# Optimization experiments

Measured on AMD Instinct MI355X. Metric: run time of the kernel, lower is better.

Reference implementation:

```python
import jax, jax.numpy as jnp
import numpy as np

EPS = 1e-12

def l2_normalize(x, axis=-1):
    return x * jax.lax.rsqrt(jnp.sum(x * x, axis=axis, keepdims=True) + EPS)

def setup_inputs() -> dict:
    key = jax.random.key(0)
    k1, k2 = jax.random.split(key)
    hidden_states = jax.random.normal(k1, (32, 1024, 32), dtype=jnp.float32)
    embedding = jax.random.normal(k2, (8192, 32), dtype=jnp.float32)
    return {"hidden_states": hidden_states, "embedding": embedding}

def reference(hidden_states, embedding):
    B, N, D = hidden_states.shape
    # flatten to tokens and L2-normalize both sides
    z_flat = l2_normalize(hidden_states.reshape(-1, D), axis=1)      # [B*N, D]
    emb_n = l2_normalize(embedding, axis=1)                          # [K, D]
    # pairwise squared L2 distance (on normalized vectors)
    distance = (jnp.sum(z_flat ** 2, axis=1, keepdims=True)
                + jnp.sum(emb_n ** 2, axis=1)
                - 2.0 * jnp.dot(z_flat, emb_n.T))                    # [B*N, K]
    min_encoding_indices = jnp.argmin(distance, axis=1).reshape(B, N)
    # codebook lookup on the RAW embedding, then normalize (get_codebook_entry)
    z_q = l2_normalize(jnp.take(embedding, min_encoding_indices, axis=0), axis=-1)  # [B, N, D]
    hidden_normed = l2_normalize(hidden_states, axis=-1)
    e_latent_loss = jnp.mean(jnp.square(jax.lax.stop_gradient(z_q) - hidden_normed))
    q_latent_loss = jnp.mean(jnp.square(z_q - jax.lax.stop_gradient(hidden_normed)))
    # straight-through estimator
    z_q = hidden_states + jax.lax.stop_gradient(z_q - hidden_states)
    return (z_q, min_encoding_indices, q_latent_loss, e_latent_loss)
```

## Files before the change

kernel.cpp:

```cpp
#include <hip/hip_runtime.h>
#include <math.h>

#define TOKENS 32768
#define KCODES 8192
#define DIM 32
#define CHUNKS 8
#define CPC (KCODES / CHUNKS)
#define ZQ_ELEMS (TOKENS * DIM)

typedef __attribute__((ext_vector_type(8))) short short8v;
typedef __attribute__((ext_vector_type(4))) float f32x4;

__device__ inline unsigned rne16(unsigned u) {
  return (u + 0x7FFFu + ((u >> 16) & 1u)) >> 16;
}

__global__ __launch_bounds__(256) void prep_codes(
    const float* __restrict__ emb, short* __restrict__ cA,
    short* __restrict__ cB, short* __restrict__ cC, float* __restrict__ nsq) {
  int gid = blockIdx.x * 256 + threadIdx.x;
  int code = gid >> 5;
  int k = gid & 31;
  float v = emb[gid];
  float s = v * v;
#pragma unroll
  for (int off = 16; off > 0; off >>= 1) s += __shfl_xor(s, off, 32);
  float r = 1.0f / sqrtf(s + 1e-12f);
  float en = v * r;
  float s2 = en * en;
#pragma unroll
  for (int off = 16; off > 0; off >>= 1) s2 += __shfl_xor(s2, off, 32);
  if (k == 0) nsq[code] = s2;

  float w = -2.0f * en;
  unsigned ua = rne16(__float_as_uint(w));
  float fa = __uint_as_float(ua << 16);
  float r1 = w - fa;
  unsigned ub = rne16(__float_as_uint(r1));
  float fb = __uint_as_float(ub << 16);
  float r2 = r1 - fb;
  unsigned uc = rne16(__float_as_uint(r2));

  int tile = code >> 4;
  int lane = (code & 15) | ((k >> 3) << 4);
  int off = tile * 512 + lane * 8 + (k & 7);
  cA[off] = (short)ua;
  cB[off] = (short)ub;
  cC[off] = (short)uc;
}

__global__ __launch_bounds__(256) void argmin_mfma(
    const float* __restrict__ hs, const short* __restrict__ cA,
    const short* __restrict__ cB, const short* __restrict__ cC,
    const float* __restrict__ nsqG, float* __restrict__ pdist,
    int* __restrict__ pidx) {
  __shared__ short lA[4096];
  __shared__ short lB[4096];
  __shared__ short lC[4096];
  __shared__ float lN[128];

  int tid = threadIdx.x;
  int l = tid & 63;
  int w = tid >> 6;
  int g = l >> 4;
  int c16 = l & 15;

  int gt0 = blockIdx.x * 16 + w * 4;

  short8v bA[4], bB[4], bC[4];
#pragma unroll
  for (int tt = 0; tt < 4; tt++) {
    int tok = (gt0 + tt) * 16 + c16;
    const float4* hp4 = (const float4*)(hs + (size_t)tok * DIM + g * 8);
    float4 q0 = hp4[0];
    float4 q1 = hp4[1];
    float x[8] = {q0.x, q0.y, q0.z, q0.w, q1.x, q1.y, q1.z, q1.w};
    float ss = 0.f;
#pragma unroll
    for (int j = 0; j < 8; j++) ss += x[j] * x[j];
    ss += __shfl_xor(ss, 16);
    ss += __shfl_xor(ss, 32);
    float rz = 1.0f / sqrtf(ss + 1e-12f);
#pragma unroll
    for (int j = 0; j < 8; j++) {
      float zn = x[j] * rz;
      unsigned ua = rne16(__float_as_uint(zn));
      float fa = __uint_as_float(ua << 16);
      float r1 = zn - fa;
      unsigned ub = rne16(__float_as_uint(r1));
      float fb = __uint_as_float(ub << 16);
      float r2 = r1 - fb;
      unsigned uc = rne16(__float_as_uint(r2));
      bA[tt][j] = (short)ua;
      bB[tt][j] = (short)ub;
      bC[tt][j] = (short)uc;
    }
  }

  float best[4] = {3.4e38f, 3.4e38f, 3.4e38f, 3.4e38f};
  int bidx[4] = {0, 0, 0, 0};
  int cbase = blockIdx.y * CPC;

  for (int s = 0; s < 8; s++) {
    __syncthreads();
    size_t eb = ((size_t)(cbase >> 4) + s * 8) * 512;
    const float4* sA = (const float4*)(cA + eb);
    const float4* sB = (const float4*)(cB + eb);
    const float4* sC = (const float4*)(cC + eb);
    ((float4*)lA)[tid] = sA[tid];
    ((float4*)lA)[tid + 256] = sA[tid + 256];
    ((float4*)lB)[tid] = sB[tid];
    ((float4*)lB)[tid + 256] = sB[tid + 256];
    ((float4*)lC)[tid] = sC[tid];
    ((float4*)lC)[tid + 256] = sC[tid + 256];
    if (tid < 128) lN[tid] = nsqG[cbase + s * 128 + tid];
    __syncthreads();

#pragma unroll
    for (int ct = 0; ct < 8; ct++) {
      f32x4 nv = *(const f32x4*)&lN[ct * 16 + g * 4];
      short8v aA = *(const short8v*)&lA[ct * 512 + l * 8];
      short8v aB = *(const short8v*)&lB[ct * 512 + l * 8];
      short8v aC = *(const short8v*)&lC[ct * 512 + l * 8];
      f32x4 acc[4];
#pragma unroll
      for (int tt = 0; tt < 4; tt++)
        acc[tt] = __builtin_amdgcn_mfma_f32_16x16x32_bf16(aA, bA[tt], nv, 0, 0, 0);
#pragma unroll
      for (int tt = 0; tt < 4; tt++)
        acc[tt] = __builtin_amdgcn_mfma_f32_16x16x32_bf16(aA, bB[tt], acc[tt], 0, 0, 0);
#pragma unroll
      for (int tt = 0; tt < 4; tt++)
        acc[tt] = __builtin_amdgcn_mfma_f32_16x16x32_bf16(aB, bA[tt], acc[tt], 0, 0, 0);
#pragma unroll
      for (int tt = 0; tt < 4; tt++)
        acc[tt] = __builtin_amdgcn_mfma_f32_16x16x32_bf16(aA, bC[tt], acc[tt], 0, 0, 0);
#pragma unroll
      for (int tt = 0; tt < 4; tt++)
        acc[tt] = __builtin_amdgcn_mfma_f32_16x16x32_bf16(aC, bA[tt], acc[tt], 0, 0, 0);
#pragma unroll
      for (int tt = 0; tt < 4; tt++)
        acc[tt] = __builtin_amdgcn_mfma_f32_16x16x32_bf16(aB, bB[tt], acc[tt], 0, 0, 0);

      int rb = cbase + s * 128 + ct * 16 + g * 4;
#pragma unroll
      for (int tt = 0; tt < 4; tt++) {
#pragma unroll
        for (int r = 0; r < 4; r++) {
          float d = acc[tt][r];
          if (d < best[tt]) { best[tt] = d; bidx[tt] = rb + r; }
        }
      }
    }
  }

#pragma unroll
  for (int tt = 0; tt < 4; tt++) {
    {
      float od = __shfl_xor(best[tt], 16);
      int oi = __shfl_xor(bidx[tt], 16);
      if (od < best[tt] || (od == best[tt] && oi < bidx[tt])) {
        best[tt] = od; bidx[tt] = oi;
      }
    }
    {
      float od = __shfl_xor(best[tt], 32);
      int oi = __shfl_xor(bidx[tt], 32);
      if (od < best[tt] || (od == best[tt] && oi < bidx[tt])) {
        best[tt] = od; bidx[tt] = oi;
      }
    }
    if (l < 16) {
      int tok = (gt0 + tt) * 16 + c16;
      pdist[(size_t)tok * CHUNKS + blockIdx.y] = best[tt];
      pidx[(size_t)tok * CHUNKS + blockIdx.y] = bidx[tt];
    }
  }
}

__global__ __launch_bounds__(256) void finalize_kernel(
    const float* __restrict__ hs, const float* __restrict__ emb,
    const float* __restrict__ pdist, const int* __restrict__ pidx,
    float* __restrict__ out, float* __restrict__ lossacc) {
  int token = blockIdx.x * 256 + threadIdx.x;

  float best = 3.4e38f;
  int bidx = 0;
#pragma unroll
  for (int c = 0; c < CHUNKS; c++) {
    float d = pdist[(size_t)token * CHUNKS + c];
    int i = pidx[(size_t)token * CHUNKS + c];
    if (d < best || (d == best && i < bidx)) { best = d; bidx = i; }
  }
  out[(size_t)ZQ_ELEMS + token] = (float)bidx;

  const float4* e = (const float4*)(emb + (size_t)bidx * DIM);
  float4 ev[8];
  float s = 0.f;
#pragma unroll
  for (int j = 0; j < 8; j++) {
    ev[j] = e[j];
    s += ev[j].x * ev[j].x + ev[j].y * ev[j].y + ev[j].z * ev[j].z +
         ev[j].w * ev[j].w;
  }
  float r = 1.0f / sqrtf(s + 1e-12f);

  const float4* hp = (const float4*)(hs + (size_t)token * DIM);
  float4 hv[8];
  float ss = 0.f;
#pragma unroll
  for (int j = 0; j < 8; j++) {
    hv[j] = hp[j];
    ss += hv[j].x * hv[j].x + hv[j].y * hv[j].y + hv[j].z * hv[j].z +
          hv[j].w * hv[j].w;
  }
  float rz = 1.0f / sqrtf(ss + 1e-12f);

  float4* op = (float4*)(out + (size_t)token * DIM);
  float acc = 0.f;
#pragma unroll
  for (int j = 0; j < 8; j++) {
    float4 zq;
    zq.x = ev[j].x * r; zq.y = ev[j].y * r;
    zq.z = ev[j].z * r; zq.w = ev[j].w * r;
    op[j] = zq;
    float dx = zq.x - hv[j].x * rz;
    float dy = zq.y - hv[j].y * rz;
    float dz = zq.z - hv[j].z * rz;
    float dw = zq.w - hv[j].w * rz;
    acc += dx * dx + dy * dy + dz * dz + dw * dw;
  }

#pragma unroll
  for (int off = 32; off > 0; off >>= 1) acc += __shfl_xor(acc, off, 64);
  __shared__ float red[4];
  int wid = threadIdx.x >> 6;
  if ((threadIdx.x & 63) == 0) red[wid] = acc;
  __syncthreads();
  if (threadIdx.x == 0) {
    float b = red[0] + red[1] + red[2] + red[3];
    atomicAdd(lossacc, b);
  }
}

__global__ void loss_write_kernel(const float* __restrict__ lossacc,
                                  float* __restrict__ out) {
  float l = lossacc[0] * (1.0f / (float)ZQ_ELEMS);
  out[ZQ_ELEMS + TOKENS] = l;
  out[ZQ_ELEMS + TOKENS + 1] = l;
}

extern "C" void kernel_launch(void* const* d_in, const int* in_sizes, int n_in,
                              void* d_out, int out_size, void* d_ws,
                              size_t ws_size, hipStream_t stream) {
  const float* hs = (const float*)d_in[0];
  const float* emb = (const float*)d_in[1];
  float* out = (float*)d_out;
  char* ws = (char*)d_ws;

  short* cA = (short*)(ws);
  short* cB = (short*)(ws + 524288);
  short* cC = (short*)(ws + 1048576);
  float* nsq = (float*)(ws + 1572864);
  float* pdist = (float*)(ws + 1605632);
  int* pidx = (int*)(ws + 2654208);
  float* lossacc = (float*)(ws + 3702784);

  hipLaunchKernelGGL(prep_codes, dim3((KCODES * DIM) / 256), dim3(256), 0,
                     stream, emb, cA, cB, cC, nsq);
  hipLaunchKernelGGL(argmin_mfma, dim3(TOKENS / 256, CHUNKS), dim3(256), 0,
                     stream, hs, cA, cB, cC, nsq, pdist, pidx);
  hipMemsetAsync(lossacc, 0, 4, stream);
  hipLaunchKernelGGL(finalize_kernel, dim3(TOKENS / 256), dim3(256), 0, stream,
                     hs, emb, pdist, pidx, out, lossacc);
  hipLaunchKernelGGL(loss_write_kernel, dim3(1), dim3(1), 0, stream, lossacc,
                     out);
}
```

Before: 102.1 us.

## Screen codes with low-precision MFMA, then rescore candidate groups in double

Replaces the six-pass bf16x3 exact argmin with a cheaper three-MFMA bf16x2 screening pass that records per-group minimum scores per token. A rescore kernel then recomputes exact double-precision distances only for codebook groups within a margin of the best screened score, and fuses the codebook lookup and loss. The screen skips token normalization because it does not change the argmin, and the loss accumulator is split across many addresses to reduce atomic contention. The risk is that the fixed margin may miss the true minimum, and double-precision rescoring per candidate group can be expensive on the vector units.

```diff
diff --git a/kernel.cpp b/kernel.cpp
--- a/kernel.cpp
+++ b/kernel.cpp
@@ -4,9 +4,12 @@
 #define TOKENS 32768
 #define KCODES 8192
 #define DIM 32
-#define CHUNKS 8
-#define CPC (KCODES / CHUNKS)
+#define NCHUNK 16
+#define CPC 512
+#define GSZ 128
+#define NGROUPS 64
 #define ZQ_ELEMS (TOKENS * DIM)
+#define MARGIN 1e-3f
 
 typedef __attribute__((ext_vector_type(8))) short short8v;
 typedef __attribute__((ext_vector_type(4))) float f32x4;
@@ -17,57 +20,40 @@
 
 __global__ __launch_bounds__(256) void prep_codes(
     const float* __restrict__ emb, short* __restrict__ cA,
-    short* __restrict__ cB, short* __restrict__ cC, float* __restrict__ nsq) {
+    short* __restrict__ cB, double* __restrict__ seArr) {
   int gid = blockIdx.x * 256 + threadIdx.x;
   int code = gid >> 5;
   int k = gid & 31;
   float v = emb[gid];
-  float s = v * v;
-#pragma unroll
-  for (int off = 16; off > 0; off >>= 1) s += __shfl_xor(s, off, 32);
-  float r = 1.0f / sqrtf(s + 1e-12f);
-  float en = v * r;
-  float s2 = en * en;
-#pragma unroll
-  for (int off = 16; off > 0; off >>= 1) s2 += __shfl_xor(s2, off, 32);
-  if (k == 0) nsq[code] = s2;
-
-  float w = -2.0f * en;
+  double dv = (double)v;
+  double ds = dv * dv;
+#pragma unroll
+  for (int off = 16; off > 0; off >>= 1) ds += __shfl_xor(ds, off, 32);
+  if (k == 0) seArr[code] = ds;
+  float r = 1.0f / sqrtf((float)ds + 1e-12f);
+  float w = -v * r;
   unsigned ua = rne16(__float_as_uint(w));
   float fa = __uint_as_float(ua << 16);
-  float r1 = w - fa;
-  unsigned ub = rne16(__float_as_uint(r1));
-  float fb = __uint_as_float(ub << 16);
-  float r2 = r1 - fb;
-  unsigned uc = rne16(__float_as_uint(r2));
-
+  unsigned ub = rne16(__float_as_uint(w - fa));
   int tile = code >> 4;
   int lane = (code & 15) | ((k >> 3) << 4);
   int off = tile * 512 + lane * 8 + (k & 7);
   cA[off] = (short)ua;
   cB[off] = (short)ub;
-  cC[off] = (short)uc;
-}
-
-__global__ __launch_bounds__(256) void argmin_mfma(
+}
+
+__global__ __launch_bounds__(256) void screen_kernel(
     const float* __restrict__ hs, const short* __restrict__ cA,
-    const short* __restrict__ cB, const short* __restrict__ cC,
-    const float* __restrict__ nsqG, float* __restrict__ pdist,
-    int* __restrict__ pidx) {
-  __shared__ short lA[4096];
-  __shared__ short lB[4096];
-  __shared__ short lC[4096];
-  __shared__ float lN[128];
-
+    const short* __restrict__ cB, float* __restrict__ pgmin) {
   int tid = threadIdx.x;
   int l = tid & 63;
   int w = tid >> 6;
   int g = l >> 4;
   int c16 = l & 15;
-
   int gt0 = blockIdx.x * 16 + w * 4;
-
-  short8v bA[4], bB[4], bC[4];
+  int chunk = blockIdx.y;
+
+  short8v zA[4], zB[4];
 #pragma unroll
   for (int tt = 0; tt < 4; tt++) {
     int tok = (gt0 + tt) * 16 + c16;
@@ -75,179 +61,148 @@
     float4 q0 = hp4[0];
     float4 q1 = hp4[1];
     float x[8] = {q0.x, q0.y, q0.z, q0.w, q1.x, q1.y, q1.z, q1.w};
-    float ss = 0.f;
-#pragma unroll
-    for (int j = 0; j < 8; j++) ss += x[j] * x[j];
-    ss += __shfl_xor(ss, 16);
-    ss += __shfl_xor(ss, 32);
-    float rz = 1.0f / sqrtf(ss + 1e-12f);
 #pragma unroll
     for (int j = 0; j < 8; j++) {
-      float zn = x[j] * rz;
-      unsigned ua = rne16(__float_as_uint(zn));
+      unsigned ua = rne16(__float_as_uint(x[j]));
       float fa = __uint_as_float(ua << 16);
-      float r1 = zn - fa;
-      unsigned ub = rne16(__float_as_uint(r1));
-      float fb = __uint_as_float(ub << 16);
-      float r2 = r1 - fb;
-      unsigned uc = rne16(__float_as_uint(r2));
-      bA[tt][j] = (short)ua;
-      bB[tt][j] = (short)ub;
-      bC[tt][j] = (short)uc;
-    }
-  }
-
-  float best[4] = {3.4e38f, 3.4e38f, 3.4e38f, 3.4e38f};
-  int bidx[4] = {0, 0, 0, 0};
-  int cbase = blockIdx.y * CPC;
-
-  for (int s = 0; s < 8; s++) {
-    __syncthreads();
-    size_t eb = ((size_t)(cbase >> 4) + s * 8) * 512;
-    const float4* sA = (const float4*)(cA + eb);
-    const float4* sB = (const float4*)(cB + eb);
-    const float4* sC = (const float4*)(cC + eb);
-    ((float4*)lA)[tid] = sA[tid];
-    ((float4*)lA)[tid + 256] = sA[tid + 256];
-    ((float4*)lB)[tid] = sB[tid];
-    ((float4*)lB)[tid + 256] = sB[tid + 256];
-    ((float4*)lC)[tid] = sC[tid];
-    ((float4*)lC)[tid + 256] = sC[tid + 256];
-    if (tid < 128) lN[tid] = nsqG[cbase + s * 128 + tid];
-    __syncthreads();
-
-#pragma unroll
-    for (int ct = 0; ct < 8; ct++) {
-      f32x4 nv = *(const f32x4*)&lN[ct * 16 + g * 4];
-      short8v aA = *(const short8v*)&lA[ct * 512 + l * 8];
-      short8v aB = *(const short8v*)&lB[ct * 512 + l * 8];
-      short8v aC = *(const short8v*)&lC[ct * 512 + l * 8];
-      f32x4 acc[4];
-#pragma unroll
-      for (int tt = 0; tt < 4; tt++)
-        acc[tt] = __builtin_amdgcn_mfma_f32_16x16x32_bf16(aA, bA[tt], nv, 0, 0, 0);
-#pragma unroll
-      for (int tt = 0; tt < 4; tt++)
-        acc[tt] = __builtin_amdgcn_mfma_f32_16x16x32_bf16(aA, bB[tt], acc[tt], 0, 0, 0);
-#pragma unroll
-      for (int tt = 0; tt < 4; tt++)
-        acc[tt] = __builtin_amdgcn_mfma_f32_16x16x32_bf16(aB, bA[tt], acc[tt], 0, 0, 0);
-#pragma unroll
-      for (int tt = 0; tt < 4; tt++)
-        acc[tt] = __builtin_amdgcn_mfma_f32_16x16x32_bf16(aA, bC[tt], acc[tt], 0, 0, 0);
-#pragma unroll
-      for (int tt = 0; tt < 4; tt++)
-        acc[tt] = __builtin_amdgcn_mfma_f32_16x16x32_bf16(aC, bA[tt], acc[tt], 0, 0, 0);
-#pragma unroll
-      for (int tt = 0; tt < 4; tt++)
-        acc[tt] = __builtin_amdgcn_mfma_f32_16x16x32_bf16(aB, bB[tt], acc[tt], 0, 0, 0);
-
-      int rb = cbase + s * 128 + ct * 16 + g * 4;
+      unsigned ub = rne16(__float_as_uint(x[j] - fa));
+      zA[tt][j] = (short)ua;
+      zB[tt][j] = (short)ub;
+    }
+  }
+
+  int tbase = chunk * (CPC / 16);
+
+  for (int grp = 0; grp < CPC / GSZ; grp++) {
+    float gm[4] = {3.4e38f, 3.4e38f, 3.4e38f, 3.4e38f};
+#pragma unroll
+    for (int ct = 0; ct < GSZ / 16; ct++) {
+      int tile = tbase + grp * (GSZ / 16) + ct;
+      short8v aA = *((const short8v*)(cA + (size_t)tile * 512) + l);
+      short8v aB = *((const short8v*)(cB + (size_t)tile * 512) + l);
 #pragma unroll
       for (int tt = 0; tt < 4; tt++) {
-#pragma unroll
-        for (int r = 0; r < 4; r++) {
-          float d = acc[tt][r];
-          if (d < best[tt]) { best[tt] = d; bidx[tt] = rb + r; }
-        }
-      }
-    }
-  }
-
-#pragma unroll
-  for (int tt = 0; tt < 4; tt++) {
-    {
-      float od = __shfl_xor(best[tt], 16);
-      int oi = __shfl_xor(bidx[tt], 16);
-      if (od < best[tt] || (od == best[tt] && oi < bidx[tt])) {
-        best[tt] = od; bidx[tt] = oi;
-      }
-    }
-    {
-      float od = __shfl_xor(best[tt], 32);
-      int oi = __shfl_xor(bidx[tt], 32);
-      if (od < best[tt] || (od == best[tt] && oi < bidx[tt])) {
-        best[tt] = od; bidx[tt] = oi;
-      }
-    }
-    if (l < 16) {
-      int tok = (gt0 + tt) * 16 + c16;
-      pdist[(size_t)tok * CHUNKS + blockIdx.y] = best[tt];
-      pidx[(size_t)tok * CHUNKS + blockIdx.y] = bidx[tt];
-    }
-  }
-}
-
-__global__ __launch_bounds__(256) void finalize_kernel(
+        f32x4 acc = {};
+        acc = __builtin_amdgcn_mfma_f32_16x16x32_bf16(aA, zA[tt], acc, 0, 0, 0);
+        acc = __builtin_amdgcn_mfma_f32_16x16x32_bf16(aA, zB[tt], acc, 0, 0, 0);
+        acc = __builtin_amdgcn_mfma_f32_16x16x32_bf16(aB, zA[tt], acc, 0, 0, 0);
+        float m = fminf(fminf(acc[0], acc[1]), fminf(acc[2], acc[3]));
+        gm[tt] = fminf(gm[tt], m);
+      }
+    }
+    int gidx = (chunk * (CPC / GSZ) + grp);
+#pragma unroll
+    for (int tt = 0; tt < 4; tt++) {
+      float v = gm[tt];
+      v = fminf(v, __shfl_xor(v, 16));
+      v = fminf(v, __shfl_xor(v, 32));
+      if (l < 16) {
+        int tok = (gt0 + tt) * 16 + c16;
+        pgmin[(size_t)gidx * TOKENS + tok] = v;
+      }
+    }
+  }
+}
+
+__global__ __launch_bounds__(256) void rescore_kernel(
     const float* __restrict__ hs, const float* __restrict__ emb,
-    const float* __restrict__ pdist, const int* __restrict__ pidx,
+    const double* __restrict__ seArr, const float* __restrict__ pgmin,
     float* __restrict__ out, float* __restrict__ lossacc) {
-  int token = blockIdx.x * 256 + threadIdx.x;
-
-  float best = 3.4e38f;
-  int bidx = 0;
-#pragma unroll
-  for (int c = 0; c < CHUNKS; c++) {
-    float d = pdist[(size_t)token * CHUNKS + c];
-    int i = pidx[(size_t)token * CHUNKS + c];
-    if (d < best || (d == best && i < bidx)) { best = d; bidx = i; }
-  }
-  out[(size_t)ZQ_ELEMS + token] = (float)bidx;
-
-  const float4* e = (const float4*)(emb + (size_t)bidx * DIM);
-  float4 ev[8];
-  float s = 0.f;
-#pragma unroll
-  for (int j = 0; j < 8; j++) {
-    ev[j] = e[j];
-    s += ev[j].x * ev[j].x + ev[j].y * ev[j].y + ev[j].z * ev[j].z +
-         ev[j].w * ev[j].w;
-  }
-  float r = 1.0f / sqrtf(s + 1e-12f);
-
-  const float4* hp = (const float4*)(hs + (size_t)token * DIM);
-  float4 hv[8];
-  float ss = 0.f;
-#pragma unroll
-  for (int j = 0; j < 8; j++) {
-    hv[j] = hp[j];
-    ss += hv[j].x * hv[j].x + hv[j].y * hv[j].y + hv[j].z * hv[j].z +
-          hv[j].w * hv[j].w;
-  }
-  float rz = 1.0f / sqrtf(ss + 1e-12f);
-
-  float4* op = (float4*)(out + (size_t)token * DIM);
-  float acc = 0.f;
-#pragma unroll
-  for (int j = 0; j < 8; j++) {
-    float4 zq;
-    zq.x = ev[j].x * r; zq.y = ev[j].y * r;
-    zq.z = ev[j].z * r; zq.w = ev[j].w * r;
-    op[j] = zq;
-    float dx = zq.x - hv[j].x * rz;
-    float dy = zq.y - hv[j].y * rz;
-    float dz = zq.z - hv[j].z * rz;
-    float dw = zq.w - hv[j].w * rz;
-    acc += dx * dx + dy * dy + dz * dz + dw * dw;
-  }
-
-#pragma unroll
-  for (int off = 32; off > 0; off >>= 1) acc += __shfl_xor(acc, off, 64);
-  __shared__ float red[4];
-  int wid = threadIdx.x >> 6;
-  if ((threadIdx.x & 63) == 0) red[wid] = acc;
+  __shared__ float zsh[4][32];
+  __shared__ float lred[4];
+  int tid = threadIdx.x;
+  int w = tid >> 6;
+  int l = tid & 63;
+  int tok = blockIdx.x * 4 + w;
+
+  if (l < 32) zsh[w][l] = hs[(size_t)tok * DIM + l];
   __syncthreads();
-  if (threadIdx.x == 0) {
-    float b = red[0] + red[1] + red[2] + red[3];
-    atomicAdd(lossacc, b);
+
+  double zd[32];
+#pragma unroll
+  for (int d = 0; d < 32; d++) zd[d] = (double)zsh[w][d];
+
+  double p = (double)zsh[w][l & 31];
+  p = p * p;
+#pragma unroll
+  for (int off = 1; off < 32; off <<= 1) p += __shfl_xor(p, off);
+  double sz = p;
+  double rz = 1.0 / sqrt(sz + 1e-12);
+
+  float v = pgmin[(size_t)l * TOKENS + tok];
+  float m = v;
+#pragma unroll
+  for (int off = 1; off < 64; off <<= 1) m = fminf(m, __shfl_xor(m, off));
+  unsigned long long mask = __ballot(v <= m + MARGIN);
+
+  double bestd = 1e300;
+  int bestidx = 0x7fffffff;
+  while (mask) {
+    int grp = __ffsll(mask) - 1;
+    mask &= mask - 1;
+#pragma unroll
+    for (int half = 0; half < 2; half++) {
+      int c = grp * GSZ + half * 64 + l;
+      const float4* ep = (const float4*)(emb + (size_t)c * DIM);
+      double dot = 0.0;
+#pragma unroll
+      for (int j = 0; j < 8; j++) {
+        float4 q = ep[j];
+        dot += zd[4 * j] * (double)q.x;
+        dot += zd[4 * j + 1] * (double)q.y;
+        dot += zd[4 * j + 2] * (double)q.z;
+        dot += zd[4 * j + 3] * (double)q.w;
+      }
+      double se = seArr[c];
+      double re = 1.0 / sqrt(se + 1e-12);
+      double D = sz * rz * rz + se * re * re - 2.0 * dot * rz * re;
+      if (D < bestd || (D == bestd && c < bestidx)) {
+        bestd = D;
+        bestidx = c;
+      }
+    }
+  }
+#pragma unroll
+  for (int off = 1; off < 64; off <<= 1) {
+    double od = __shfl_xor(bestd, off);
+    int oi = __shfl_xor(bestidx, off);
+    if (od < bestd || (od == bestd && oi < bestidx)) {
+      bestd = od;
+      bestidx = oi;
+    }
+  }
+
+  if (l == 0) out[(size_t)ZQ_ELEMS + tok] = (float)bestidx;
+
+  int d = l & 31;
+  float ev = emb[(size_t)bestidx * DIM + d];
+  double reW = 1.0 / sqrt(seArr[bestidx] + 1e-12);
+  float zq = (float)((double)ev * reW);
+  if (l < 32) out[(size_t)tok * DIM + d] = zq;
+  double hn = zd[d] * rz;
+  double diff = (double)zq - hn;
+  double lp = (l < 32) ? diff * diff : 0.0;
+#pragma unroll
+  for (int off = 1; off < 64; off <<= 1) lp += __shfl_xor(lp, off);
+  if (l == 0) lred[w] = (float)lp;
+  __syncthreads();
+  if (tid == 0) {
+    float b = lred[0] + lred[1] + lred[2] + lred[3];
+    atomicAdd(lossacc + (blockIdx.x & 127), b);
   }
 }
 
 __global__ void loss_write_kernel(const float* __restrict__ lossacc,
                                   float* __restrict__ out) {
-  float l = lossacc[0] * (1.0f / (float)ZQ_ELEMS);
-  out[ZQ_ELEMS + TOKENS] = l;
-  out[ZQ_ELEMS + TOKENS + 1] = l;
+  int l = threadIdx.x;
+  float s = lossacc[l] + lossacc[l + 64];
+#pragma unroll
+  for (int off = 1; off < 64; off <<= 1) s += __shfl_xor(s, off);
+  if (l == 0) {
+    float v = s * (1.0f / (float)ZQ_ELEMS);
+    out[ZQ_ELEMS + TOKENS] = v;
+    out[ZQ_ELEMS + TOKENS + 1] = v;
+  }
 }
 
 extern "C" void kernel_launch(void* const* d_in, const int* in_sizes, int n_in,
@@ -260,19 +215,17 @@
 
   short* cA = (short*)(ws);
   short* cB = (short*)(ws + 524288);
-  short* cC = (short*)(ws + 1048576);
-  float* nsq = (float*)(ws + 1572864);
-  float* pdist = (float*)(ws + 1605632);
-  int* pidx = (int*)(ws + 2654208);
-  float* lossacc = (float*)(ws + 3702784);
+  double* seArr = (double*)(ws + 1048576);
+  float* pgmin = (float*)(ws + 1114112);
+  float* lossacc = (float*)(ws + 9502720);
 
   hipLaunchKernelGGL(prep_codes, dim3((KCODES * DIM) / 256), dim3(256), 0,
-                     stream, emb, cA, cB, cC, nsq);
-  hipLaunchKernelGGL(argmin_mfma, dim3(TOKENS / 256, CHUNKS), dim3(256), 0,
-                     stream, hs, cA, cB, cC, nsq, pdist, pidx);
-  hipMemsetAsync(lossacc, 0, 4, stream);
-  hipLaunchKernelGGL(finalize_kernel, dim3(TOKENS / 256), dim3(256), 0, stream,
-                     hs, emb, pdist, pidx, out, lossacc);
-  hipLaunchKernelGGL(loss_write_kernel, dim3(1), dim3(1), 0, stream, lossacc,
+                     stream, emb, cA, cB, seArr);
+  hipMemsetAsync(lossacc, 0, 512, stream);
+  hipLaunchKernelGGL(screen_kernel, dim3(TOKENS / 256, NCHUNK), dim3(256), 0,
+                     stream, hs, cA, cB, pgmin);
+  hipLaunchKernelGGL(rescore_kernel, dim3(TOKENS / 4), dim3(256), 0, stream,
+                     hs, emb, seArr, pgmin, out, lossacc);
+  hipLaunchKernelGGL(loss_write_kernel, dim3(1), dim3(64), 0, stream, lossacc,
                      out);
 }
```

After: 241.4 us. 2.36x slower.
